# Performance work log

Hardware: AMD Instinct MI355X
Metric: run time of the kernel (lower is better)

Reference implementation:

```python
import jax, jax.numpy as jnp
import numpy as np

TEMPERATURE = 0.05
EPS = 1e-8  # torch.nn.CosineSimilarity eps


def setup_inputs() -> dict:
    key = jax.random.key(0)
    k1, k2 = jax.random.split(key)
    z1 = jax.random.normal(k1, (8192, 512), dtype=jnp.float32)
    z2 = jax.random.normal(k2, (8192, 512), dtype=jnp.float32)
    return {"z1": z1, "z2": z2}


def reference(z1, z2):
    # Pairwise cosine similarity via GEMM on raw dots / outer product of norms,
    # matching torch CosineSimilarity: dot / max(||a||*||b||, eps).
    dots = jnp.einsum('id,jd->ij', z1, z2)          # [N, N]
    n1 = jnp.linalg.norm(z1, axis=-1)               # [N]
    n2 = jnp.linalg.norm(z2, axis=-1)               # [N]
    denom = jnp.maximum(n1[:, None] * n2[None, :], EPS)
    sim = dots / denom / TEMPERATURE                # [N, N]
    return -jnp.mean(jax.scipy.special.logsumexp(sim, axis=-1))
```

## Files before the change

kernel.cpp:

```cpp
#include <hip/hip_runtime.h>
#include <hip/hip_bf16.h>

#define NROW 8192
#define DDIM 512
#define TEMP_INV 20.0f
#define SHIFT 20.0f

#define BM 256
#define BN 256
#define BK 64
#define KT (DDIM / BK)
#define TILE_A_ELE (BM * BK)
#define BUF_ELE (2 * TILE_A_ELE)
#define LDS_BYTES (2 * BUF_ELE * 2)

typedef __attribute__((ext_vector_type(8))) short short8;
typedef __attribute__((ext_vector_type(4))) float f32x4;

__device__ __forceinline__ void gload16(const __hip_bfloat16* g, __hip_bfloat16* l) {
  __builtin_amdgcn_global_load_lds(
      (const __attribute__((address_space(1))) void*)g,
      (__attribute__((address_space(3))) void*)l,
      16, 0, 0);
}

__global__ __launch_bounds__(256) void normalize_rows(
    const float* __restrict__ z1, const float* __restrict__ z2,
    __hip_bfloat16* __restrict__ z1n, __hip_bfloat16* __restrict__ z2n,
    float* __restrict__ rowsum) {
  int row = blockIdx.x * 4 + (threadIdx.x >> 6);
  int lane = threadIdx.x & 63;

  const float* src;
  __hip_bfloat16* dst;
  float numer;
  if (row < NROW) {
    src = z1 + (size_t)row * DDIM;
    dst = z1n + (size_t)row * DDIM;
    numer = TEMP_INV;
    if (lane == 0) rowsum[row] = 0.0f;
  } else {
    int r = row - NROW;
    src = z2 + (size_t)r * DDIM;
    dst = z2n + (size_t)r * DDIM;
    numer = 1.0f;
  }

  float4 v0 = *reinterpret_cast<const float4*>(src + lane * 8);
  float4 v1 = *reinterpret_cast<const float4*>(src + lane * 8 + 4);
  float ss = v0.x * v0.x + v0.y * v0.y + v0.z * v0.z + v0.w * v0.w +
             v1.x * v1.x + v1.y * v1.y + v1.z * v1.z + v1.w * v1.w;
#pragma unroll
  for (int off = 32; off; off >>= 1) ss += __shfl_xor(ss, off);

  float scale = numer / fmaxf(sqrtf(ss), 1e-8f);

  float vals[8] = {v0.x, v0.y, v0.z, v0.w, v1.x, v1.y, v1.z, v1.w};
  union { __hip_bfloat16 h[8]; uint4 q; } pk;
#pragma unroll
  for (int j = 0; j < 8; ++j) pk.h[j] = __float2bfloat16(vals[j] * scale);
  *reinterpret_cast<uint4*>(dst + lane * 8) = pk.q;
}

#define MFMA_Q(A_, B_, QM, QN)                                                 \
  do {                                                                         \
    __builtin_amdgcn_s_setprio(1);                                             \
    _Pragma("unroll") for (int mi = 0; mi < 4; ++mi) {                         \
      _Pragma("unroll") for (int ni = 0; ni < 2; ++ni) {                       \
        _Pragma("unroll") for (int kk = 0; kk < 2; ++kk) {                     \
          acc[(QM) * 4 + mi][(QN) * 2 + ni] =                                  \
              __builtin_amdgcn_mfma_f32_16x16x32_bf16(                         \
                  (A_)[mi * 2 + kk], (B_)[ni * 2 + kk],                        \
                  acc[(QM) * 4 + mi][(QN) * 2 + ni], 0, 0, 0);                 \
        }                                                                      \
      }                                                                        \
    }                                                                          \
    __builtin_amdgcn_s_setprio(0);                                             \
  } while (0)

#define BAR_PRE()                                                \
  do {                                                           \
    __builtin_amdgcn_s_barrier();                                \
    asm volatile("s_waitcnt lgkmcnt(0)" ::: "memory");           \
    __builtin_amdgcn_sched_barrier(0);                           \
  } while (0)

#define BAR_POST() __builtin_amdgcn_s_barrier()

#define VMC(N) asm volatile("s_waitcnt vmcnt(" #N ")" ::: "memory")

__global__ __launch_bounds__(512, 2) void gemm_lse(
    const __hip_bfloat16* __restrict__ An,
    const __hip_bfloat16* __restrict__ Bn,
    float* __restrict__ rowsum) {
  extern __shared__ __align__(16) __hip_bfloat16 lds[];

  const int bid = blockIdx.x;
  const int chunk = bid & 7;
  const int slot = bid >> 3;
  const int by = chunk * 4 + ((slot >> 2) & 3);
  const int bx = (slot >> 4) * 4 + (slot & 3);
  const int brow = by * BM;
  const int bcol = bx * BN;

  const int tid = threadIdx.x;
  const int w = tid >> 6;
  const int lane = tid & 63;
  const int wr = w >> 2;
  const int wc = w & 3;

  f32x4 acc[8][4];
#pragma unroll
  for (int m = 0; m < 8; ++m)
#pragma unroll
    for (int n = 0; n < 4; ++n) acc[m][n] = (f32x4)0.0f;

  const int srow8 = lane >> 3;
  const int sslot = (lane & 7) ^ srow8;

  auto STAGE_HALF = [&](int st, int h) {
    const int stm = st & (KT - 1);
    const __hip_bfloat16* gbase =
        (h < 2) ? An + (size_t)brow * DDIM : Bn + (size_t)bcol * DDIM;
    const int rowt = (h & 1) * 128 + w * 16;
    const __hip_bfloat16* g =
        gbase + (size_t)(rowt + srow8) * DDIM + stm * BK + sslot * 8;
    __hip_bfloat16* dst = lds + (size_t)(stm & 1) * BUF_ELE +
                          ((h >= 2) ? TILE_A_ELE : 0) + rowt * BK;
    gload16(g, dst);
    gload16(g + (size_t)8 * DDIM, dst + 8 * BK);
  };

  const int hi = lane >> 4;
  const int l15 = lane & 15;
  const int x7 = lane & 7;

  auto READ_A = [&](short8* dst, int bufb, int qm) {
#pragma unroll
    for (int mi = 0; mi < 4; ++mi)
#pragma unroll
      for (int kk = 0; kk < 2; ++kk) {
        int row = wr * 128 + qm * 64 + mi * 16 + l15;
        int sl = ((kk * 4 + hi) ^ x7) * 8;
        dst[mi * 2 + kk] = *reinterpret_cast<const short8*>(
            &lds[(size_t)bufb * BUF_ELE + row * BK + sl]);
      }
  };
  auto READ_B = [&](short8* dst, int bufb, int qn) {
#pragma unroll
    for (int ni = 0; ni < 2; ++ni)
#pragma unroll
      for (int kk = 0; kk < 2; ++kk) {
        int row = wc * 64 + qn * 32 + ni * 16 + l15;
        int sl = ((kk * 4 + hi) ^ x7) * 8;
        dst[ni * 2 + kk] = *reinterpret_cast<const short8*>(
            &lds[(size_t)bufb * BUF_ELE + TILE_A_ELE + row * BK + sl]);
      }
  };

  STAGE_HALF(0, 0); STAGE_HALF(0, 1); STAGE_HALF(0, 2); STAGE_HALF(0, 3);
  STAGE_HALF(1, 0);
  VMC(2);
  __builtin_amdgcn_s_barrier();
  __builtin_amdgcn_sched_barrier(0);

  short8 af[8], bf0[4], bf1[4];

#pragma unroll
  for (int i = 0; i < KT / 2; ++i) {
    READ_A(af, 0, 0); READ_B(bf0, 0, 0);
    STAGE_HALF(2 * i + 1, 1);
    BAR_PRE();  MFMA_Q(af, bf0, 0, 0);  BAR_POST();
    READ_B(bf1, 0, 1);
    STAGE_HALF(2 * i + 1, 2);
    BAR_PRE();  MFMA_Q(af, bf1, 0, 1);  BAR_POST();
    READ_A(af, 0, 1);
    STAGE_HALF(2 * i + 1, 3);
    BAR_PRE();  MFMA_Q(af, bf0, 1, 0);  BAR_POST();
    STAGE_HALF(2 * i + 2, 0);
    VMC(2);
    BAR_PRE();  MFMA_Q(af, bf1, 1, 1);  BAR_POST();
    READ_A(af, 1, 0); READ_B(bf0, 1, 0);
    STAGE_HALF(2 * i + 2, 1);
    BAR_PRE();  MFMA_Q(af, bf0, 0, 0);  BAR_POST();
    READ_B(bf1, 1, 1);
    STAGE_HALF(2 * i + 2, 2);
    BAR_PRE();  MFMA_Q(af, bf1, 0, 1);  BAR_POST();
    READ_A(af, 1, 1);
    STAGE_HALF(2 * i + 2, 3);
    BAR_PRE();  MFMA_Q(af, bf0, 1, 0);  BAR_POST();
    STAGE_HALF(2 * i + 3, 0);
    VMC(2);
    BAR_PRE();  MFMA_Q(af, bf1, 1, 1);  BAR_POST();
  }

  const float L2E = 1.4426950408889634f;
  const float NEG = -SHIFT * 1.4426950408889634f;
#pragma unroll
  for (int m = 0; m < 8; ++m) {
#pragma unroll
    for (int r = 0; r < 4; ++r) {
      float s = 0.0f;
#pragma unroll
      for (int n = 0; n < 4; ++n)
        s += exp2f(fmaf(acc[m][n][r], L2E, NEG));
      s += __shfl_xor(s, 1);
      s += __shfl_xor(s, 2);
      s += __shfl_xor(s, 4);
      s += __shfl_xor(s, 8);
      if (l15 == 0)
        atomicAdd(&rowsum[brow + wr * 128 + m * 16 + hi * 4 + r], s);
    }
  }
}

__global__ __launch_bounds__(1024) void finalize_lse(
    const float* __restrict__ rowsum, float* __restrict__ out) {
  __shared__ float sm[16];
  float s = 0.0f;
  for (int i = threadIdx.x; i < NROW; i += 1024) s += logf(rowsum[i]);
#pragma unroll
  for (int off = 32; off; off >>= 1) s += __shfl_xor(s, off);
  int w = threadIdx.x >> 6;
  if ((threadIdx.x & 63) == 0) sm[w] = s;
  __syncthreads();
  if (threadIdx.x == 0) {
    float t = 0.0f;
#pragma unroll
    for (int i = 0; i < 16; ++i) t += sm[i];
    out[0] = -(t / (float)NROW + SHIFT);
  }
}

extern "C" void kernel_launch(void* const* d_in, const int* in_sizes, int n_in,
                              void* d_out, int out_size, void* d_ws,
                              size_t ws_size, hipStream_t stream) {
  const float* z1 = (const float*)d_in[0];
  const float* z2 = (const float*)d_in[1];
  float* out = (float*)d_out;

  char* ws = (char*)d_ws;
  __hip_bfloat16* z1n = (__hip_bfloat16*)ws;
  __hip_bfloat16* z2n = (__hip_bfloat16*)(ws + (size_t)NROW * DDIM * 2);
  float* rowsum = (float*)(ws + (size_t)2 * NROW * DDIM * 2);

  static bool attr_set = false;
  if (!attr_set) {
    hipFuncSetAttribute((const void*)gemm_lse,
                        hipFuncAttributeMaxDynamicSharedMemorySize, LDS_BYTES);
    attr_set = true;
  }

  normalize_rows<<<dim3((2 * NROW) / 4), dim3(256), 0, stream>>>(z1, z2, z1n,
                                                                 z2n, rowsum);
  gemm_lse<<<dim3((NROW / BM) * (NROW / BN)), dim3(512), LDS_BYTES, stream>>>(
      z1n, z2n, rowsum);
  finalize_lse<<<dim3(1), dim3(1024), 0, stream>>>(rowsum, out);
}
```

Measured before the change: 162.3 us.

## Restructure GEMM main loop phases to prefetch B fragments and drop explicit lgkmcnt waits

Rewrites the K-loop as macro phases. The bf0 fragments for the next buffer are now prefetched during the last MFMA block of the previous phase, and the explicit lgkmcnt(0) wait before each barrier is gone, so the compiler inserts finer-grained waits. A fragment loads are split around the global-to-LDS stage issue. The outer loop loses its unroll pragma. The aim is to overlap LDS reads with MFMA work and cut stalls, at the risk of register pressure, changed scheduling, and LDS hazards if the barrier ordering is wrong.

```diff
diff --git a/kernel.cpp b/kernel.cpp
--- a/kernel.cpp
+++ b/kernel.cpp
@@ -62,32 +62,83 @@
   *reinterpret_cast<uint4*>(dst + lane * 8) = pk.q;
 }
 
-#define MFMA_Q(A_, B_, QM, QN)                                                 \
-  do {                                                                         \
-    __builtin_amdgcn_s_setprio(1);                                             \
-    _Pragma("unroll") for (int mi = 0; mi < 4; ++mi) {                         \
-      _Pragma("unroll") for (int ni = 0; ni < 2; ++ni) {                       \
-        _Pragma("unroll") for (int kk = 0; kk < 2; ++kk) {                     \
-          acc[(QM) * 4 + mi][(QN) * 2 + ni] =                                  \
-              __builtin_amdgcn_mfma_f32_16x16x32_bf16(                         \
-                  (A_)[mi * 2 + kk], (B_)[ni * 2 + kk],                        \
-                  acc[(QM) * 4 + mi][(QN) * 2 + ni], 0, 0, 0);                 \
-        }                                                                      \
-      }                                                                        \
-    }                                                                          \
-    __builtin_amdgcn_s_setprio(0);                                             \
-  } while (0)
-
-#define BAR_PRE()                                                \
-  do {                                                           \
-    __builtin_amdgcn_s_barrier();                                \
-    asm volatile("s_waitcnt lgkmcnt(0)" ::: "memory");           \
-    __builtin_amdgcn_sched_barrier(0);                           \
-  } while (0)
-
-#define BAR_POST() __builtin_amdgcn_s_barrier()
-
 #define VMC(N) asm volatile("s_waitcnt vmcnt(" #N ")" ::: "memory")
+#define SBAR()                          \
+  do {                                  \
+    __builtin_amdgcn_s_barrier();       \
+    __builtin_amdgcn_sched_barrier(0);  \
+  } while (0)
+
+#define LDSA(BUFB, QM, MI, KK)                                                \
+  (*reinterpret_cast<const short8*>(                                          \
+      &lds[(size_t)(BUFB) * BUF_ELE +                                         \
+           (wr * 128 + (QM) * 64 + (MI) * 16 + l15) * BK +                    \
+           ((((KK) * 4 + hi) ^ x7) * 8)]))
+#define LDSB(BUFB, QN, NI, KK)                                                \
+  (*reinterpret_cast<const short8*>(                                          \
+      &lds[(size_t)(BUFB) * BUF_ELE + TILE_A_ELE +                            \
+           (wc * 64 + (QN) * 32 + (NI) * 16 + l15) * BK +                     \
+           ((((KK) * 4 + hi) ^ x7) * 8)]))
+
+#define MF4(QM, MI, QN, BF)                                                   \
+  acc[(QM) * 4 + (MI)][(QN) * 2 + 0] =                                        \
+      __builtin_amdgcn_mfma_f32_16x16x32_bf16(                                \
+          af[(MI) * 2 + 0], (BF)[0], acc[(QM) * 4 + (MI)][(QN) * 2 + 0],      \
+          0, 0, 0);                                                           \
+  acc[(QM) * 4 + (MI)][(QN) * 2 + 0] =                                        \
+      __builtin_amdgcn_mfma_f32_16x16x32_bf16(                                \
+          af[(MI) * 2 + 1], (BF)[1], acc[(QM) * 4 + (MI)][(QN) * 2 + 0],      \
+          0, 0, 0);                                                           \
+  acc[(QM) * 4 + (MI)][(QN) * 2 + 1] =                                        \
+      __builtin_amdgcn_mfma_f32_16x16x32_bf16(                                \
+          af[(MI) * 2 + 0], (BF)[2], acc[(QM) * 4 + (MI)][(QN) * 2 + 1],      \
+          0, 0, 0);                                                           \
+  acc[(QM) * 4 + (MI)][(QN) * 2 + 1] =                                        \
+      __builtin_amdgcn_mfma_f32_16x16x32_bf16(                                \
+          af[(MI) * 2 + 1], (BF)[3], acc[(QM) * 4 + (MI)][(QN) * 2 + 1],      \
+          0, 0, 0);
+
+#define PHASE_A(BUFB, QM, ST, H)                                              \
+  do {                                                                        \
+    af[0] = LDSA(BUFB, QM, 0, 0); af[1] = LDSA(BUFB, QM, 0, 1);               \
+    af[2] = LDSA(BUFB, QM, 1, 0); af[3] = LDSA(BUFB, QM, 1, 1);               \
+    STAGE_HALF(ST, H);                                                        \
+    af[4] = LDSA(BUFB, QM, 2, 0); af[5] = LDSA(BUFB, QM, 2, 1);               \
+    af[6] = LDSA(BUFB, QM, 3, 0); af[7] = LDSA(BUFB, QM, 3, 1);               \
+    SBAR();                                                                   \
+    __builtin_amdgcn_s_setprio(1);                                            \
+    MF4(QM, 0, 0, bf0) MF4(QM, 1, 0, bf0)                                     \
+    MF4(QM, 2, 0, bf0) MF4(QM, 3, 0, bf0)                                     \
+    __builtin_amdgcn_s_setprio(0);                                            \
+    SBAR();                                                                   \
+  } while (0)
+
+#define PHASE_B(BUFB, ST, H)                                                  \
+  do {                                                                        \
+    bf1[0] = LDSB(BUFB, 1, 0, 0); bf1[1] = LDSB(BUFB, 1, 0, 1);               \
+    bf1[2] = LDSB(BUFB, 1, 1, 0); bf1[3] = LDSB(BUFB, 1, 1, 1);               \
+    STAGE_HALF(ST, H);                                                        \
+    SBAR();                                                                   \
+    __builtin_amdgcn_s_setprio(1);                                            \
+    MF4(0, 0, 1, bf1) MF4(0, 1, 1, bf1)                                       \
+    MF4(0, 2, 1, bf1) MF4(0, 3, 1, bf1)                                       \
+    __builtin_amdgcn_s_setprio(0);                                            \
+    SBAR();                                                                   \
+  } while (0)
+
+#define PHASE_W(ST, PBUF)                                                     \
+  do {                                                                        \
+    STAGE_HALF(ST, 0);                                                        \
+    VMC(2);                                                                   \
+    SBAR();                                                                   \
+    bf0[0] = LDSB(PBUF, 0, 0, 0); bf0[1] = LDSB(PBUF, 0, 0, 1);               \
+    bf0[2] = LDSB(PBUF, 0, 1, 0); bf0[3] = LDSB(PBUF, 0, 1, 1);               \
+    __builtin_amdgcn_s_setprio(1);                                            \
+    MF4(1, 0, 1, bf1) MF4(1, 1, 1, bf1)                                       \
+    MF4(1, 2, 1, bf1) MF4(1, 3, 1, bf1)                                       \
+    __builtin_amdgcn_s_setprio(0);                                            \
+    SBAR();                                                                   \
+  } while (0)
 
 __global__ __launch_bounds__(512, 2) void gemm_lse(
     const __hip_bfloat16* __restrict__ An,
@@ -135,63 +186,25 @@
   const int l15 = lane & 15;
   const int x7 = lane & 7;
 
-  auto READ_A = [&](short8* dst, int bufb, int qm) {
-#pragma unroll
-    for (int mi = 0; mi < 4; ++mi)
-#pragma unroll
-      for (int kk = 0; kk < 2; ++kk) {
-        int row = wr * 128 + qm * 64 + mi * 16 + l15;
-        int sl = ((kk * 4 + hi) ^ x7) * 8;
-        dst[mi * 2 + kk] = *reinterpret_cast<const short8*>(
-            &lds[(size_t)bufb * BUF_ELE + row * BK + sl]);
-      }
-  };
-  auto READ_B = [&](short8* dst, int bufb, int qn) {
-#pragma unroll
-    for (int ni = 0; ni < 2; ++ni)
-#pragma unroll
-      for (int kk = 0; kk < 2; ++kk) {
-        int row = wc * 64 + qn * 32 + ni * 16 + l15;
-        int sl = ((kk * 4 + hi) ^ x7) * 8;
-        dst[ni * 2 + kk] = *reinterpret_cast<const short8*>(
-            &lds[(size_t)bufb * BUF_ELE + TILE_A_ELE + row * BK + sl]);
-      }
-  };
-
   STAGE_HALF(0, 0); STAGE_HALF(0, 1); STAGE_HALF(0, 2); STAGE_HALF(0, 3);
   STAGE_HALF(1, 0);
   VMC(2);
-  __builtin_amdgcn_s_barrier();
-  __builtin_amdgcn_sched_barrier(0);
+  SBAR();
 
   short8 af[8], bf0[4], bf1[4];
-
-#pragma unroll
+  bf0[0] = LDSB(0, 0, 0, 0); bf0[1] = LDSB(0, 0, 0, 1);
+  bf0[2] = LDSB(0, 0, 1, 0); bf0[3] = LDSB(0, 0, 1, 1);
+
   for (int i = 0; i < KT / 2; ++i) {
-    READ_A(af, 0, 0); READ_B(bf0, 0, 0);
-    STAGE_HALF(2 * i + 1, 1);
-    BAR_PRE();  MFMA_Q(af, bf0, 0, 0);  BAR_POST();
-    READ_B(bf1, 0, 1);
-    STAGE_HALF(2 * i + 1, 2);
-    BAR_PRE();  MFMA_Q(af, bf1, 0, 1);  BAR_POST();
-    READ_A(af, 0, 1);
-    STAGE_HALF(2 * i + 1, 3);
-    BAR_PRE();  MFMA_Q(af, bf0, 1, 0);  BAR_POST();
-    STAGE_HALF(2 * i + 2, 0);
-    VMC(2);
-    BAR_PRE();  MFMA_Q(af, bf1, 1, 1);  BAR_POST();
-    READ_A(af, 1, 0); READ_B(bf0, 1, 0);
-    STAGE_HALF(2 * i + 2, 1);
-    BAR_PRE();  MFMA_Q(af, bf0, 0, 0);  BAR_POST();
-    READ_B(bf1, 1, 1);
-    STAGE_HALF(2 * i + 2, 2);
-    BAR_PRE();  MFMA_Q(af, bf1, 0, 1);  BAR_POST();
-    READ_A(af, 1, 1);
-    STAGE_HALF(2 * i + 2, 3);
-    BAR_PRE();  MFMA_Q(af, bf0, 1, 0);  BAR_POST();
-    STAGE_HALF(2 * i + 3, 0);
-    VMC(2);
-    BAR_PRE();  MFMA_Q(af, bf1, 1, 1);  BAR_POST();
+    const int t1 = 2 * i + 1, t2 = 2 * i + 2, t3 = 2 * i + 3;
+    PHASE_A(0, 0, t1, 1);
+    PHASE_B(0, t1, 2);
+    PHASE_A(0, 1, t1, 3);
+    PHASE_W(t2, 1);
+    PHASE_A(1, 0, t2, 1);
+    PHASE_B(1, t2, 2);
+    PHASE_A(1, 1, t2, 3);
+    PHASE_W(t3, 0);
   }
 
   const float L2E = 1.4426950408889634f;
```

Measured after the change: 160.2 us. Within noise of the previous version (-1.3%).
